# Kernel tuning notes

Measured on AMD Instinct MI355X. Metric: run time of the kernel, lower is better.

Reference implementation:

```python
import jax, jax.numpy as jnp
import numpy as np

B, S, E = 4, 2048, 1024
H, D = 16, 64  # n_heads, head_dim; scale hardcoded as 1/sqrt(64) in source


def setup_inputs() -> dict:
    key = jax.random.key(0)
    ks = jax.random.split(key, 6)
    mk = lambda k, shp, scale=1.0: (jax.random.normal(k, shp, dtype=jnp.float32) * scale)
    return {
        "queries": mk(ks[0], (B, S, E)),
        "keys": mk(ks[1], (B, S, E)),
        "values": mk(ks[2], (B, S, E)),
        "Wq": mk(ks[3], (E, H * D), E ** -0.5),
        "Wk": mk(ks[4], (E, H * D), E ** -0.5),
        "Wv": mk(ks[5], (E, H * D), E ** -0.5),
    }


def reference(queries, keys, values, Wq, Wk, Wv):
    # linear projections
    q = jnp.einsum("bse,ef->bsf", queries, Wq).reshape(B, S, H, D)
    k = jnp.einsum("bse,ef->bsf", keys, Wk).reshape(B, S, H, D)
    v = jnp.einsum("bse,ef->bsf", values, Wv).reshape(B, S, H, D)
    # scaled dot-product attention per head (scale hardcoded to 1/sqrt(64) in source)
    scores = jnp.einsum("bqhd,bkhd->bhqk", q, k) * (1.0 / np.sqrt(64.0)).astype(np.float32)
    weights = jax.nn.softmax(scores, axis=-1)
    ctx = jnp.einsum("bhqk,bkhd->bqhd", weights, v)
    # merge heads back: [B, S, H*D]
    return ctx.reshape(B, S, H * D)
```

## Files before the change

kernel.cpp:

```cpp
#include <hip/hip_runtime.h>
#include <math.h>

#define SEQ 2048
#define EMB 1024
#define NH 16
#define HD 64
#define BH 64
#define L2E 1.44269504088896340736f

typedef __attribute__((ext_vector_type(8))) short bf16x8;
typedef __attribute__((ext_vector_type(4))) float f32x4;
typedef __attribute__((ext_vector_type(16))) float f32x16;
typedef __attribute__((ext_vector_type(4))) unsigned short u16x4;

__device__ __forceinline__ unsigned short f2bf(float f) {
  union { float fv; unsigned u; } v; v.fv = f;
  return (unsigned short)((v.u + 0x7FFFu + ((v.u >> 16) & 1u)) >> 16);
}

__device__ __forceinline__ unsigned cvt_pk_bf16(float lo, float hi) {
  unsigned r;
  asm("v_cvt_pk_bf16_f32 %0, %1, %2" : "=v"(r) : "v"(lo), "v"(hi));
  return r;
}

__device__ __forceinline__ void gl_lds16(const void* g, void* l) {
  __builtin_amdgcn_global_load_lds(
      (const __attribute__((address_space(1))) unsigned*)g,
      (__attribute__((address_space(3))) unsigned*)l, 16, 0, 0);
}

__global__ __launch_bounds__(256) void k_cvt(const float* __restrict__ x0,
                                             const float* __restrict__ x1,
                                             const float* __restrict__ x2,
                                             unsigned short* __restrict__ y0,
                                             unsigned short* __restrict__ y1,
                                             unsigned short* __restrict__ y2) {
  const int NC = (4 * SEQ * EMB) / 8;
  for (int i = blockIdx.x * blockDim.x + threadIdx.x; i < NC;
       i += gridDim.x * blockDim.x) {
#pragma unroll
    for (int t = 0; t < 3; ++t) {
      const float* x = (t == 0) ? x0 : (t == 1) ? x1 : x2;
      unsigned short* y = (t == 0) ? y0 : (t == 1) ? y1 : y2;
      f32x4 lo = *(const f32x4*)(x + (size_t)i * 8);
      f32x4 hi = *(const f32x4*)(x + (size_t)i * 8 + 4);
      union { unsigned u[4]; bf16x8 v; } pk;
      pk.u[0] = cvt_pk_bf16(lo[0], lo[1]);
      pk.u[1] = cvt_pk_bf16(lo[2], lo[3]);
      pk.u[2] = cvt_pk_bf16(hi[0], hi[1]);
      pk.u[3] = cvt_pk_bf16(hi[2], hi[3]);
      *(bf16x8*)(y + (size_t)i * 8) = pk.v;
    }
  }
}

__global__ __launch_bounds__(256) void k_wt3(const float* __restrict__ Wq,
                                             const float* __restrict__ Wk,
                                             const float* __restrict__ Wv,
                                             unsigned short* __restrict__ tq,
                                             unsigned short* __restrict__ tk,
                                             unsigned short* __restrict__ tv) {
  int z = blockIdx.z;
  const float* W = (z == 0) ? Wq : (z == 1) ? Wk : Wv;
  unsigned short* Wt = (z == 0) ? tq : (z == 1) ? tk : tv;
  const float scale = (z == 0) ? 0.125f * L2E : 1.0f;

  __shared__ float tile[32][33];
  int j0 = blockIdx.x * 32, i0 = blockIdx.y * 32;
  int tx = threadIdx.x & 31, ty = threadIdx.x >> 5;
#pragma unroll
  for (int r = 0; r < 32; r += 8)
    tile[ty + r][tx] = W[(i0 + ty + r) * EMB + j0 + tx];
  __syncthreads();
#pragma unroll
  for (int r = 0; r < 32; r += 8)
    Wt[(j0 + ty + r) * EMB + i0 + tx] = f2bf(tile[tx][ty + r] * scale);
}

__global__ __launch_bounds__(256) void k_proj(
    const unsigned short* __restrict__ xq, const unsigned short* __restrict__ xk,
    const unsigned short* __restrict__ xv,
    const unsigned short* __restrict__ w0, const unsigned short* __restrict__ w1,
    const unsigned short* __restrict__ w2,
    unsigned short* __restrict__ o0, unsigned short* __restrict__ o1,
    unsigned short* __restrict__ o2) {
  int z = blockIdx.z;
  const unsigned short* X = (z == 0) ? xq : (z == 1) ? xk : xv;
  const unsigned short* Wt = (z == 0) ? w0 : (z == 1) ? w1 : w2;
  unsigned short* O = (z == 0) ? o0 : (z == 1) ? o1 : o2;

  __shared__ __align__(16) unsigned short As[2][128 * 64];
  __shared__ __align__(16) unsigned short Bs[2][128 * 64];

  int tid = threadIdx.x;
  int lane = tid & 63, w = tid >> 6;
  int ln15 = lane & 15, lg = lane >> 4;
  int wr = w >> 1, wc = w & 1;
  int row0 = blockIdx.x * 128, col0 = blockIdx.y * 128;

  const char* Xb = (const char*)X;
  const char* Wb = (const char*)Wt;

  f32x4 acc[4][4];
#pragma unroll
  for (int i = 0; i < 4; ++i)
#pragma unroll
    for (int j = 0; j < 4; ++j) acc[i][j] = (f32x4){0.f, 0.f, 0.f, 0.f};

  int so[4];
#pragma unroll
  for (int c = 0; c < 4; ++c) {
    int o = w * 4096 + c * 1024 + lane * 16;
    so[c] = o ^ (((o >> 7) & 7) << 4);
  }

  auto stage = [&](int buf, int kt) {
#pragma unroll
    for (int c = 0; c < 4; ++c) {
      gl_lds16(Xb + (size_t)(row0 + (so[c] >> 7)) * (EMB * 2) + kt * 128 + (so[c] & 127),
               (char*)As[buf] + w * 4096 + c * 1024);
      gl_lds16(Wb + (size_t)(col0 + (so[c] >> 7)) * (EMB * 2) + kt * 128 + (so[c] & 127),
               (char*)Bs[buf] + w * 4096 + c * 1024);
    }
  };

  stage(0, 0);
  __syncthreads();

  for (int kt = 0; kt < 16; ++kt) {
    int cur = kt & 1;
    if (kt < 15) stage(cur ^ 1, kt + 1);

#pragma unroll
    for (int ks = 0; ks < 2; ++ks) {
      bf16x8 a[4], bb[4];
#pragma unroll
      for (int i = 0; i < 4; ++i) {
        int row = wr * 64 + i * 16 + ln15;
        int ba = (row * 128 + ks * 64 + lg * 16) ^ ((row & 7) << 4);
        a[i] = *(const bf16x8*)((const char*)As[cur] + ba);
      }
#pragma unroll
      for (int j = 0; j < 4; ++j) {
        int row = wc * 64 + j * 16 + ln15;
        int ba = (row * 128 + ks * 64 + lg * 16) ^ ((row & 7) << 4);
        bb[j] = *(const bf16x8*)((const char*)Bs[cur] + ba);
      }
      __builtin_amdgcn_s_setprio(1);
#pragma unroll
      for (int i = 0; i < 4; ++i)
#pragma unroll
        for (int j = 0; j < 4; ++j)
          acc[i][j] = __builtin_amdgcn_mfma_f32_16x16x32_bf16(a[i], bb[j], acc[i][j], 0, 0, 0);
      __builtin_amdgcn_s_setprio(0);
    }
    __syncthreads();
  }

  if (z == 2) {
#pragma unroll
    for (int i = 0; i < 4; ++i) {
#pragma unroll
      for (int j = 0; j < 4; ++j) {
        int col = col0 + wc * 64 + j * 16 + ln15;
        int h = col >> 6, d = col & 63;
        int rowb = row0 + wr * 64 + i * 16 + lg * 4;
        int b = rowb >> 11, s = rowb & (SEQ - 1);
        u16x4 hv;
#pragma unroll
        for (int r = 0; r < 4; ++r) hv[r] = f2bf(acc[i][j][r]);
        *(u16x4*)&O[(((size_t)(b * NH + h) * HD) + d) * SEQ + s] = hv;
      }
    }
  } else {
#pragma unroll
    for (int i = 0; i < 4; ++i) {
#pragma unroll
      for (int j = 0; j < 4; ++j) {
#pragma unroll
        for (int r = 0; r < 4; ++r) {
          int row = row0 + wr * 64 + i * 16 + lg * 4 + r;
          int col = col0 + wc * 64 + j * 16 + ln15;
          int b = row >> 11, s = row & (SEQ - 1);
          int h = col >> 6, d = col & 63;
          O[(((size_t)(b * NH + h) * SEQ) + s) * HD + d] = f2bf(acc[i][j][r]);
        }
      }
    }
  }
}

__global__ __launch_bounds__(512) void k_attn(const unsigned short* __restrict__ Q,
                                              const unsigned short* __restrict__ K,
                                              const unsigned short* __restrict__ Vt,
                                              float* __restrict__ out) {
  __shared__ __align__(16) unsigned short Klds[2 * 32 * 64];
  __shared__ __align__(16) unsigned short Vlds[2 * 64 * 64];

  const int id = blockIdx.x;
  const int swz = (id & 7) * 64 + (id >> 3);
  const int bh = swz >> 3, qb = swz & 7;
  const int b = bh >> 4, h = bh & 15;

  const int tid = threadIdx.x;
  const int w = tid >> 6, lane = tid & 63;
  const int q31 = lane & 31;
  const int hi = lane >> 5;
  const int q0 = qb * 256 + w * 32;

  const unsigned short* Qb = Q + (size_t)bh * SEQ * HD;
  const char* Kb = (const char*)(K + (size_t)bh * SEQ * HD);
  const char* Vb = (const char*)(Vt + (size_t)bh * HD * SEQ);

  bf16x8 qf[4];
#pragma unroll
  for (int kk = 0; kk < 4; ++kk)
    qf[kk] = *(const bf16x8*)&Qb[(q0 + q31) * HD + kk * 16 + hi * 8];

  f32x16 ctx[2];
#pragma unroll
  for (int db = 0; db < 2; ++db)
#pragma unroll
    for (int r = 0; r < 16; ++r) ctx[db][r] = 0.f;
  float l_loc = 0.f;

  f32x16 zero16;
#pragma unroll
  for (int r = 0; r < 16; ++r) zero16[r] = 0.f;

  const int sw = (q31 & 7) << 4;
  int kaddr[4];
#pragma unroll
  for (int kk = 0; kk < 4; ++kk)
    kaddr[kk] = q31 * 128 + (((kk * 32) | (hi * 16)) ^ sw);
  int vaddr[2][2];
#pragma unroll
  for (int pi = 0; pi < 2; ++pi)
#pragma unroll
    for (int j = 0; j < 2; ++j)
      vaddr[pi][j] = q31 * 128 + (((pi * 64) | (j * 32) | (hi * 16)) ^ sw);

  const int o0 = w * 1024 + lane * 16;
  const int os0 = o0 ^ (((o0 >> 7) & 7) << 4);

  auto stageK = [&](int slot, int kt) {
    if (w < 4)
      gl_lds16(Kb + (size_t)kt * 4096 + os0, (char*)Klds + slot * 4096 + w * 1024);
  };
  auto stageV = [&](int slot, int vt) {
    gl_lds16(Vb + (size_t)(os0 >> 7) * (SEQ * 2) + vt * 128 + (os0 & 127),
             (char*)Vlds + slot * 8192 + w * 1024);
  };

  auto qk = [&](f32x16& sx, const char* kbase) {
    __builtin_amdgcn_s_setprio(1);
    bf16x8 kf0 = *(const bf16x8*)(kbase + kaddr[0]);
    sx = __builtin_amdgcn_mfma_f32_32x32x16_bf16(kf0, qf[0], zero16, 0, 0, 0);
#pragma unroll
    for (int kk = 1; kk < 4; ++kk) {
      bf16x8 kf = *(const bf16x8*)(kbase + kaddr[kk]);
      sx = __builtin_amdgcn_mfma_f32_32x32x16_bf16(kf, qf[kk], sx, 0, 0, 0);
    }
    __builtin_amdgcn_s_setprio(0);
  };

  auto smpv = [&](f32x16& sx, int pinIdx, int vb) {
#pragma unroll
    for (int r = 0; r < 16; ++r) sx[r] = __builtin_amdgcn_exp2f(sx[r]);
    float sm[8];
#pragma unroll
    for (int r = 0; r < 8; ++r) sm[r] = sx[r] + sx[r + 8];
#pragma unroll
    for (int st = 4; st > 0; st >>= 1)
#pragma unroll
      for (int r = 0; r < st; ++r) sm[r] += sm[r + st];
    l_loc += sm[0];

    unsigned a0 = cvt_pk_bf16(sx[0], sx[1]);
    unsigned a1 = cvt_pk_bf16(sx[2], sx[3]);
    unsigned a2 = cvt_pk_bf16(sx[4], sx[5]);
    unsigned a3 = cvt_pk_bf16(sx[6], sx[7]);
    unsigned a4 = cvt_pk_bf16(sx[8], sx[9]);
    unsigned a5 = cvt_pk_bf16(sx[10], sx[11]);
    unsigned a6 = cvt_pk_bf16(sx[12], sx[13]);
    unsigned a7 = cvt_pk_bf16(sx[14], sx[15]);
    asm volatile("v_permlane32_swap_b32 %0, %1" : "+v"(a0), "+v"(a2));
    asm volatile("v_permlane32_swap_b32 %0, %1" : "+v"(a1), "+v"(a3));
    asm volatile("v_permlane32_swap_b32 %0, %1" : "+v"(a4), "+v"(a6));
    asm volatile("v_permlane32_swap_b32 %0, %1" : "+v"(a5), "+v"(a7));
    union { unsigned u[4]; bf16x8 v; } pa_lo, pa_hi;
    pa_lo.u[0] = a0; pa_lo.u[1] = a1; pa_lo.u[2] = a2; pa_lo.u[3] = a3;
    pa_hi.u[0] = a4; pa_hi.u[1] = a5; pa_hi.u[2] = a6; pa_hi.u[3] = a7;

    const char* vbp = (const char*)Vlds + vb;
    __builtin_amdgcn_s_setprio(1);
#pragma unroll
    for (int db = 0; db < 2; ++db) {
      bf16x8 v0 = *(const bf16x8*)(vbp + db * 4096 + vaddr[pinIdx][0]);
      bf16x8 v1 = *(const bf16x8*)(vbp + db * 4096 + vaddr[pinIdx][1]);
      ctx[db] = __builtin_amdgcn_mfma_f32_32x32x16_bf16(pa_lo.v, v0, ctx[db], 0, 0, 0);
      ctx[db] = __builtin_amdgcn_mfma_f32_32x32x16_bf16(pa_hi.v, v1, ctx[db], 0, 0, 0);
    }
    __builtin_amdgcn_s_setprio(0);
  };

  const char* K0 = (const char*)Klds;
  const char* K1 = (const char*)Klds + 4096;
  f32x16 sA, sB;

  stageK(0, 0);
  stageV(0, 0);
  __syncthreads();
  qk(sA, K0);
  stageK(1, 1);
  __syncthreads();

  for (int tp = 0; tp < 31; ++tp) {
    const int vb = (tp & 1) << 13;
    qk(sB, K1);
    stageK(0, 2 * tp + 2);
    stageV((tp + 1) & 1, tp + 1);
    smpv(sA, 0, vb);
    __syncthreads();
    qk(sA, K0);
    stageK(1, 2 * tp + 3);
    smpv(sB, 1, vb);
    __syncthreads();
  }
  qk(sB, K1);
  smpv(sA, 0, 8192);
  smpv(sB, 1, 8192);

  float lfull = l_loc + __shfl_xor(l_loc, 32);
  float linv = 1.0f / lfull;
  float lr[16];
#pragma unroll
  for (int r = 0; r < 16; ++r)
    lr[r] = __shfl(linv, (r & 3) + 8 * (r >> 2) + 4 * hi);
#pragma unroll
  for (int db = 0; db < 2; ++db) {
#pragma unroll
    for (int r = 0; r < 16; ++r) {
      int q = q0 + (r & 3) + 8 * (r >> 2) + 4 * hi;
      out[((size_t)b * SEQ + q) * (NH * HD) + h * HD + db * 32 + q31] = ctx[db][r] * lr[r];
    }
  }
}

extern "C" void kernel_launch(void* const* d_in, const int* in_sizes, int n_in,
                              void* d_out, int out_size, void* d_ws, size_t ws_size,
                              hipStream_t stream) {
  (void)in_sizes; (void)n_in; (void)out_size; (void)ws_size;
  const float* queries = (const float*)d_in[0];
  const float* keys    = (const float*)d_in[1];
  const float* values  = (const float*)d_in[2];
  const float* Wq = (const float*)d_in[3];
  const float* Wk = (const float*)d_in[4];
  const float* Wv = (const float*)d_in[5];
  float* out = (float*)d_out;

  char* ws = (char*)d_ws;
  const size_t MB = 1024 * 1024;
  unsigned short* xq_ws = (unsigned short*)(ws);
  unsigned short* xk_ws = (unsigned short*)(ws + 16 * MB);
  unsigned short* xv_ws = (unsigned short*)(ws + 32 * MB);
  unsigned short* q_ws  = (unsigned short*)(ws + 48 * MB);
  unsigned short* k_ws  = (unsigned short*)(ws + 64 * MB);
  unsigned short* v_ws  = (unsigned short*)(ws + 80 * MB);
  unsigned short* wtq   = (unsigned short*)(ws + 96 * MB);
  unsigned short* wtk   = (unsigned short*)(ws + 98 * MB);
  unsigned short* wtv   = (unsigned short*)(ws + 100 * MB);

  k_wt3<<<dim3(32, 32, 3), 256, 0, stream>>>(Wq, Wk, Wv, wtq, wtk, wtv);
  k_cvt<<<dim3(2048), 256, 0, stream>>>(queries, keys, values, xq_ws, xk_ws, xv_ws);
  k_proj<<<dim3(64, 8, 3), 256, 0, stream>>>(xq_ws, xk_ws, xv_ws,
                                             wtq, wtk, wtv, q_ws, k_ws, v_ws);
  k_attn<<<dim3(512), 512, 0, stream>>>(q_ws, k_ws, v_ws, out);
}
```

Before: 177.3 us.

## Fuse fp32-to-bf16 input conversion into projection GEMM; compute row sums via MFMA

Removes the separate conversion kernel. The projection GEMM now loads fp32 activations into registers, converts them to bf16 and writes them to swizzled LDS one tile ahead, while the weights still use direct global-to-LDS loads. This avoids writing and re-reading a bf16 copy of the inputs and saves a kernel launch, but each A-tile load is twice as wide and the LDS store moves into the main loop. Separately, the attention kernel computes the softmax denominator with two extra MFMAs against a ones vector, replacing the shuffle reductions. That adds matrix work but removes VALU adds and the final shuffles.

```diff
diff --git a/kernel.cpp b/kernel.cpp
--- a/kernel.cpp
+++ b/kernel.cpp
@@ -28,31 +28,6 @@
   __builtin_amdgcn_global_load_lds(
       (const __attribute__((address_space(1))) unsigned*)g,
       (__attribute__((address_space(3))) unsigned*)l, 16, 0, 0);
-}
-
-__global__ __launch_bounds__(256) void k_cvt(const float* __restrict__ x0,
-                                             const float* __restrict__ x1,
-                                             const float* __restrict__ x2,
-                                             unsigned short* __restrict__ y0,
-                                             unsigned short* __restrict__ y1,
-                                             unsigned short* __restrict__ y2) {
-  const int NC = (4 * SEQ * EMB) / 8;
-  for (int i = blockIdx.x * blockDim.x + threadIdx.x; i < NC;
-       i += gridDim.x * blockDim.x) {
-#pragma unroll
-    for (int t = 0; t < 3; ++t) {
-      const float* x = (t == 0) ? x0 : (t == 1) ? x1 : x2;
-      unsigned short* y = (t == 0) ? y0 : (t == 1) ? y1 : y2;
-      f32x4 lo = *(const f32x4*)(x + (size_t)i * 8);
-      f32x4 hi = *(const f32x4*)(x + (size_t)i * 8 + 4);
-      union { unsigned u[4]; bf16x8 v; } pk;
-      pk.u[0] = cvt_pk_bf16(lo[0], lo[1]);
-      pk.u[1] = cvt_pk_bf16(lo[2], lo[3]);
-      pk.u[2] = cvt_pk_bf16(hi[0], hi[1]);
-      pk.u[3] = cvt_pk_bf16(hi[2], hi[3]);
-      *(bf16x8*)(y + (size_t)i * 8) = pk.v;
-    }
-  }
 }
 
 __global__ __launch_bounds__(256) void k_wt3(const float* __restrict__ Wq,
@@ -79,14 +54,14 @@
 }
 
 __global__ __launch_bounds__(256) void k_proj(
-    const unsigned short* __restrict__ xq, const unsigned short* __restrict__ xk,
-    const unsigned short* __restrict__ xv,
+    const float* __restrict__ xq, const float* __restrict__ xk,
+    const float* __restrict__ xv,
     const unsigned short* __restrict__ w0, const unsigned short* __restrict__ w1,
     const unsigned short* __restrict__ w2,
     unsigned short* __restrict__ o0, unsigned short* __restrict__ o1,
     unsigned short* __restrict__ o2) {
   int z = blockIdx.z;
-  const unsigned short* X = (z == 0) ? xq : (z == 1) ? xk : xv;
+  const float* X = (z == 0) ? xq : (z == 1) ? xk : xv;
   const unsigned short* Wt = (z == 0) ? w0 : (z == 1) ? w1 : w2;
   unsigned short* O = (z == 0) ? o0 : (z == 1) ? o1 : o2;
 
@@ -108,29 +83,57 @@
 #pragma unroll
     for (int j = 0; j < 4; ++j) acc[i][j] = (f32x4){0.f, 0.f, 0.f, 0.f};
 
-  int so[4];
+  int oc[4], dswz[4];
+  size_t srcA[4];
 #pragma unroll
   for (int c = 0; c < 4; ++c) {
-    int o = w * 4096 + c * 1024 + lane * 16;
-    so[c] = o ^ (((o >> 7) & 7) << 4);
-  }
-
-  auto stage = [&](int buf, int kt) {
+    oc[c] = w * 4096 + c * 1024 + lane * 16;
+    dswz[c] = oc[c] ^ (((oc[c] >> 7) & 7) << 4);
+    srcA[c] = (size_t)(row0 + (oc[c] >> 7)) * (EMB * 4) +
+              (size_t)(oc[c] & 127) * 2;
+  }
+  int soB[4];
+#pragma unroll
+  for (int c = 0; c < 4; ++c) soB[c] = oc[c] ^ (((oc[c] >> 7) & 7) << 4);
+
+  f32x4 ar[4][2];
+  auto ldA = [&](int kt) {
 #pragma unroll
     for (int c = 0; c < 4; ++c) {
-      gl_lds16(Xb + (size_t)(row0 + (so[c] >> 7)) * (EMB * 2) + kt * 128 + (so[c] & 127),
-               (char*)As[buf] + w * 4096 + c * 1024);
-      gl_lds16(Wb + (size_t)(col0 + (so[c] >> 7)) * (EMB * 2) + kt * 128 + (so[c] & 127),
+      const char* p = Xb + srcA[c] + kt * 256;
+      ar[c][0] = *(const f32x4*)p;
+      ar[c][1] = *(const f32x4*)(p + 16);
+    }
+  };
+  auto wrA = [&](int buf) {
+#pragma unroll
+    for (int c = 0; c < 4; ++c) {
+      union { unsigned u[4]; bf16x8 v; } pk;
+      pk.u[0] = cvt_pk_bf16(ar[c][0][0], ar[c][0][1]);
+      pk.u[1] = cvt_pk_bf16(ar[c][0][2], ar[c][0][3]);
+      pk.u[2] = cvt_pk_bf16(ar[c][1][0], ar[c][1][1]);
+      pk.u[3] = cvt_pk_bf16(ar[c][1][2], ar[c][1][3]);
+      *(bf16x8*)((char*)As[buf] + dswz[c]) = pk.v;
+    }
+  };
+  auto stageB = [&](int buf, int kt) {
+#pragma unroll
+    for (int c = 0; c < 4; ++c)
+      gl_lds16(Wb + (size_t)(col0 + (soB[c] >> 7)) * (EMB * 2) + kt * 128 + (soB[c] & 127),
                (char*)Bs[buf] + w * 4096 + c * 1024);
-    }
-  };
-
-  stage(0, 0);
+  };
+
+  ldA(0);
+  stageB(0, 0);
+  wrA(0);
   __syncthreads();
 
   for (int kt = 0; kt < 16; ++kt) {
     int cur = kt & 1;
-    if (kt < 15) stage(cur ^ 1, kt + 1);
+    if (kt < 15) {
+      ldA(kt + 1);
+      stageB(cur ^ 1, kt + 1);
+    }
 
 #pragma unroll
     for (int ks = 0; ks < 2; ++ks) {
@@ -155,6 +158,7 @@
           acc[i][j] = __builtin_amdgcn_mfma_f32_16x16x32_bf16(a[i], bb[j], acc[i][j], 0, 0, 0);
       __builtin_amdgcn_s_setprio(0);
     }
+    if (kt < 15) wrA(cur ^ 1);
     __syncthreads();
   }
 
@@ -223,11 +227,14 @@
   for (int db = 0; db < 2; ++db)
 #pragma unroll
     for (int r = 0; r < 16; ++r) ctx[db][r] = 0.f;
-  float l_loc = 0.f;
 
   f32x16 zero16;
 #pragma unroll
   for (int r = 0; r < 16; ++r) zero16[r] = 0.f;
+  union { unsigned u[4]; bf16x8 v; } onesf;
+#pragma unroll
+  for (int r = 0; r < 4; ++r) onesf.u[r] = 0x3F803F80u;
+  f32x16 lsum = zero16;
 
   const int sw = (q31 & 7) << 4;
   int kaddr[4];
@@ -268,14 +275,6 @@
   auto smpv = [&](f32x16& sx, int pinIdx, int vb) {
 #pragma unroll
     for (int r = 0; r < 16; ++r) sx[r] = __builtin_amdgcn_exp2f(sx[r]);
-    float sm[8];
-#pragma unroll
-    for (int r = 0; r < 8; ++r) sm[r] = sx[r] + sx[r + 8];
-#pragma unroll
-    for (int st = 4; st > 0; st >>= 1)
-#pragma unroll
-      for (int r = 0; r < st; ++r) sm[r] += sm[r + st];
-    l_loc += sm[0];
 
     unsigned a0 = cvt_pk_bf16(sx[0], sx[1]);
     unsigned a1 = cvt_pk_bf16(sx[2], sx[3]);
@@ -295,6 +294,8 @@
 
     const char* vbp = (const char*)Vlds + vb;
     __builtin_amdgcn_s_setprio(1);
+    lsum = __builtin_amdgcn_mfma_f32_32x32x16_bf16(pa_lo.v, onesf.v, lsum, 0, 0, 0);
+    lsum = __builtin_amdgcn_mfma_f32_32x32x16_bf16(pa_hi.v, onesf.v, lsum, 0, 0, 0);
 #pragma unroll
     for (int db = 0; db < 2; ++db) {
       bf16x8 v0 = *(const bf16x8*)(vbp + db * 4096 + vaddr[pinIdx][0]);
@@ -332,18 +333,13 @@
   smpv(sA, 0, 8192);
   smpv(sB, 1, 8192);
 
-  float lfull = l_loc + __shfl_xor(l_loc, 32);
-  float linv = 1.0f / lfull;
-  float lr[16];
-#pragma unroll
-  for (int r = 0; r < 16; ++r)
-    lr[r] = __shfl(linv, (r & 3) + 8 * (r >> 2) + 4 * hi);
 #pragma unroll
   for (int db = 0; db < 2; ++db) {
 #pragma unroll
     for (int r = 0; r < 16; ++r) {
       int q = q0 + (r & 3) + 8 * (r >> 2) + 4 * hi;
-      out[((size_t)b * SEQ + q) * (NH * HD) + h * HD + db * 32 + q31] = ctx[db][r] * lr[r];
+      out[((size_t)b * SEQ + q) * (NH * HD) + h * HD + db * 32 + q31] =
+          ctx[db][r] / lsum[r];
     }
   }
 }
@@ -362,19 +358,15 @@
 
   char* ws = (char*)d_ws;
   const size_t MB = 1024 * 1024;
-  unsigned short* xq_ws = (unsigned short*)(ws);
-  unsigned short* xk_ws = (unsigned short*)(ws + 16 * MB);
-  unsigned short* xv_ws = (unsigned short*)(ws + 32 * MB);
-  unsigned short* q_ws  = (unsigned short*)(ws + 48 * MB);
-  unsigned short* k_ws  = (unsigned short*)(ws + 64 * MB);
-  unsigned short* v_ws  = (unsigned short*)(ws + 80 * MB);
-  unsigned short* wtq   = (unsigned short*)(ws + 96 * MB);
-  unsigned short* wtk   = (unsigned short*)(ws + 98 * MB);
-  unsigned short* wtv   = (unsigned short*)(ws + 100 * MB);
+  unsigned short* q_ws = (unsigned short*)(ws);
+  unsigned short* k_ws = (unsigned short*)(ws + 16 * MB);
+  unsigned short* v_ws = (unsigned short*)(ws + 32 * MB);
+  unsigned short* wtq  = (unsigned short*)(ws + 48 * MB);
+  unsigned short* wtk  = (unsigned short*)(ws + 50 * MB);
+  unsigned short* wtv  = (unsigned short*)(ws + 52 * MB);
 
   k_wt3<<<dim3(32, 32, 3), 256, 0, stream>>>(Wq, Wk, Wv, wtq, wtk, wtv);
-  k_cvt<<<dim3(2048), 256, 0, stream>>>(queries, keys, values, xq_ws, xk_ws, xv_ws);
-  k_proj<<<dim3(64, 8, 3), 256, 0, stream>>>(xq_ws, xk_ws, xv_ws,
+  k_proj<<<dim3(64, 8, 3), 256, 0, stream>>>(queries, keys, values,
                                              wtq, wtk, wtv, q_ws, k_ws, v_ws);
   k_attn<<<dim3(512), 512, 0, stream>>>(q_ws, k_ws, v_ws, out);
 }
```

After: 169.1 us. 4.6% less time.
